# Performance work log

Measured on AMD Instinct MI355X. Metric: run time of the kernel, lower is better.

The kernel has to match this reference:

```python
import jax, jax.numpy as jnp
import numpy as np


def setup_inputs() -> dict:
    key = jax.random.key(0)
    k1, k2, k3, k4, k5 = jax.random.split(key, 5)
    B, ENS, XDIM, YDIM = 8, 256, 8192, 256
    return {
        "Ens_ten": jax.random.normal(k1, (B, ENS, XDIM), dtype=jnp.float32),
        "H": jax.random.normal(k2, (XDIM, YDIM), dtype=jnp.float32),
        "y_true_mean": jax.random.normal(k3, (1, YDIM), dtype=jnp.float32),
        "y_true_std": jax.random.normal(k4, (1, YDIM), dtype=jnp.float32),
        "noise": jax.random.normal(k5, (B, YDIM, ENS), dtype=jnp.float32),
    }


def reference(Ens_ten, H, y_true_mean, y_true_std, noise):
    # Ens_ten: [b, ens, xdim]; H: [xdim, ydim]
    b, ens, xdim = Ens_ten.shape
    Y = jnp.einsum('bex,xy->bey', Ens_ten, H)          # observation_func (linear)
    x_m = jnp.mean(Ens_ten, axis=1, keepdims=True)     # [b,1,xdim]
    y_m = jnp.mean(Y, axis=1, keepdims=True)           # [b,1,ydim]
    Xc = jnp.swapaxes(Ens_ten - x_m, 1, 2)             # [b,xdim,ens]
    Yc = jnp.swapaxes(Y - y_m, 1, 2)                   # [b,ydim,ens]
    C_xy = jnp.einsum('bxe,bye->bxy', Xc, Yc) / ens    # [b,xdim,ydim]
    C_yy = jnp.einsum('bue,bve->buv', Yc, Yc) / ens    # [b,ydim,ydim]
    R = jnp.diag(jnp.square(y_true_std)[0])            # [ydim,ydim], broadcasts over batch
    A = R + C_yy                                       # [b,ydim,ydim]
    # torch.linalg.solve(A, C_xy, left=False): K = C_xy @ inv(A)
    K = jnp.swapaxes(
        jnp.linalg.solve(jnp.swapaxes(A, 1, 2), jnp.swapaxes(C_xy, 1, 2)), 1, 2
    )                                                  # [b,xdim,ydim]
    R_2 = noise * jnp.square(y_true_std)[:, :, None]   # [b,ydim,ens]
    innov = y_true_mean[:, :, None] - Yc + R_2         # [b,ydim,ens]
    update = jnp.einsum('bxy,bye->bxe', K, innov)      # [b,xdim,ens]
    return Ens_ten + jnp.swapaxes(update, 1, 2)
```

## Files before the change

### kernel.cpp

```cpp
#include <hip/hip_runtime.h>

#define ENSN 256
#define XDIM 8192
#define YD 256
#define BATCH 8

#define OFF_Y   0
#define OFF_YC  524288
#define OFF_AUG 1048576
#define OFF_W   2097152
#define OFF_XM  2621440

typedef __attribute__((ext_vector_type(4))) short short4v;
typedef __attribute__((ext_vector_type(8))) short short8v;
typedef __attribute__((ext_vector_type(4))) float float4v;

__device__ __forceinline__ unsigned short f2bf_rne(float x) {
    unsigned u = __float_as_uint(x);
    u += 0x7FFFu + ((u >> 16) & 1u);
    return (unsigned short)(u >> 16);
}

__global__ __launch_bounds__(256) void k1_colmean(const float* __restrict__ E,
                                                  float* __restrict__ xm) {
    int x = blockIdx.x * 256 + threadIdx.x;
    int b = blockIdx.y;
    const float* p = E + (size_t)b * ENSN * XDIM + x;
    float s = 0.f;
    #pragma unroll 8
    for (int e = 0; e < ENSN; e++) s += p[(size_t)e * XDIM];
    xm[b * XDIM + x] = s * (1.0f / ENSN);
}

__global__ __launch_bounds__(256) void kc_h(const float* __restrict__ H,
                                            short* __restrict__ Hthi,
                                            short* __restrict__ Htlo) {
    __shared__ float T[64][65];
    int k0 = blockIdx.x * 64, n0 = blockIdx.y * 64;
    int tid = threadIdx.x;
    int c = tid & 63, g = tid >> 6;
    #pragma unroll
    for (int p = 0; p < 16; p++)
        T[g + p * 4][c] = H[(size_t)(k0 + g + p * 4) * YD + n0 + c];
    __syncthreads();
    #pragma unroll
    for (int p = 0; p < 16; p++) {
        int nn = g + p * 4;
        float v = T[c][nn];
        unsigned short h = f2bf_rne(v);
        float hf = __uint_as_float(((unsigned)h) << 16);
        unsigned short l2 = f2bf_rne(v - hf);
        Hthi[(size_t)(n0 + nn) * XDIM + k0 + c] = (short)h;
        Htlo[(size_t)(n0 + nn) * XDIM + k0 + c] = (short)l2;
    }
}

#define EST 40
#define BST 40

__global__ __launch_bounds__(512, 2) void k2m_ygemm(const float* __restrict__ E,
                                                    const short* __restrict__ Hthi,
                                                    const short* __restrict__ Htlo,
                                                    float* __restrict__ Y) {
    __shared__ __align__(16) short Ehi[64 * EST];
    __shared__ __align__(16) short Elo[64 * EST];
    __shared__ __align__(16) short Bhi[256 * BST];
    __shared__ __align__(16) short Blo[256 * BST];
    int tid = threadIdx.x;
    int lane = tid & 63;
    int w = tid >> 6;
    int m0 = blockIdx.x * 64;
    int kb0 = blockIdx.y * 512;
    int wr = (w & 1) * 32;
    int wc = (w >> 1) * 64;
    float4v acc[8];
    #pragma unroll
    for (int i = 0; i < 8; i++) acc[i] = (float4v){0.f, 0.f, 0.f, 0.f};

    int erow = tid >> 3, ecol = (tid & 7) * 4;
    int brow = tid >> 1, bhalf = (tid & 1) * 16;
    int fr = lane & 15, fg = lane >> 4;

    for (int s = 0; s < 16; s++) {
        int kb = kb0 + s * 32;
        float4 ev = *(const float4*)&E[(size_t)(m0 + erow) * XDIM + kb + ecol];
        float vv[4] = {ev.x, ev.y, ev.z, ev.w};
        short4v hi4, lo4;
        #pragma unroll
        for (int j = 0; j < 4; j++) {
            unsigned short h = f2bf_rne(vv[j]);
            float hf = __uint_as_float(((unsigned)h) << 16);
            unsigned short l2 = f2bf_rne(vv[j] - hf);
            hi4[j] = (short)h; lo4[j] = (short)l2;
        }
        *(short4v*)&Ehi[erow * EST + ecol] = hi4;
        *(short4v*)&Elo[erow * EST + ecol] = lo4;
        short8v bh0 = *(const short8v*)&Hthi[(size_t)brow * XDIM + kb + bhalf];
        short8v bh1 = *(const short8v*)&Hthi[(size_t)brow * XDIM + kb + bhalf + 8];
        short8v bl0 = *(const short8v*)&Htlo[(size_t)brow * XDIM + kb + bhalf];
        short8v bl1 = *(const short8v*)&Htlo[(size_t)brow * XDIM + kb + bhalf + 8];
        *(short8v*)&Bhi[brow * BST + bhalf]     = bh0;
        *(short8v*)&Bhi[brow * BST + bhalf + 8] = bh1;
        *(short8v*)&Blo[brow * BST + bhalf]     = bl0;
        *(short8v*)&Blo[brow * BST + bhalf + 8] = bl1;
        __syncthreads();
        short8v ah[2], al[2], bhf[4], blf[4];
        #pragma unroll
        for (int ti = 0; ti < 2; ti++) {
            ah[ti] = *(const short8v*)&Ehi[(wr + ti * 16 + fr) * EST + fg * 8];
            al[ti] = *(const short8v*)&Elo[(wr + ti * 16 + fr) * EST + fg * 8];
        }
        #pragma unroll
        for (int tj = 0; tj < 4; tj++) {
            bhf[tj] = *(const short8v*)&Bhi[(wc + tj * 16 + fr) * BST + fg * 8];
            blf[tj] = *(const short8v*)&Blo[(wc + tj * 16 + fr) * BST + fg * 8];
        }
        #pragma unroll
        for (int ti = 0; ti < 2; ti++)
            #pragma unroll
            for (int tj = 0; tj < 4; tj++) {
                int a = ti * 4 + tj;
                acc[a] = __builtin_amdgcn_mfma_f32_16x16x32_bf16(ah[ti], bhf[tj], acc[a], 0, 0, 0);
                acc[a] = __builtin_amdgcn_mfma_f32_16x16x32_bf16(ah[ti], blf[tj], acc[a], 0, 0, 0);
                acc[a] = __builtin_amdgcn_mfma_f32_16x16x32_bf16(al[ti], bhf[tj], acc[a], 0, 0, 0);
            }
        __syncthreads();
    }
    #pragma unroll
    for (int ti = 0; ti < 2; ti++)
        #pragma unroll
        for (int tj = 0; tj < 4; tj++)
            #pragma unroll
            for (int q = 0; q < 4; q++) {
                int row = m0 + wr + ti * 16 + fg * 4 + q;
                int col = wc + tj * 16 + fr;
                atomicAdd(&Y[row * YD + col], acc[ti * 4 + tj][q]);
            }
}

__global__ __launch_bounds__(256) void k3_center(const float* __restrict__ Y,
                                                 const float* __restrict__ ytm,
                                                 const float* __restrict__ ystd,
                                                 const float* __restrict__ noise,
                                                 float* __restrict__ Yc,
                                                 float* __restrict__ aug) {
    int b = blockIdx.y, tid = threadIdx.x;
    int y0 = blockIdx.x * 64;
    __shared__ float red[4][64];
    __shared__ float ym[64], tms[64], s2[64];
    __shared__ float T[64][65];
    int yl = tid & 63, q = tid >> 6;
    float s = 0.f;
    for (int e = q * 64; e < q * 64 + 64; e++)
        s += Y[(size_t)(b * ENSN + e) * YD + y0 + yl];
    red[q][yl] = s;
    __syncthreads();
    if (tid < 64) {
        ym[tid] = (red[0][tid] + red[1][tid] + red[2][tid] + red[3][tid]) * (1.0f / ENSN);
        float sd = ystd[y0 + tid];
        s2[tid] = sd * sd;
        tms[tid] = ytm[y0 + tid];
    }
    __syncthreads();
    for (int e0 = 0; e0 < ENSN; e0 += 64) {
        #pragma unroll
        for (int p = 0; p < 16; p++) {
            int er = q + p * 4;
            T[er][yl] = Y[(size_t)(b * ENSN + e0 + er) * YD + y0 + yl];
        }
        __syncthreads();
        int ec = yl;
        #pragma unroll
        for (int p = 0; p < 16; p++) {
            int yr = q + p * 4;
            int y = y0 + yr, e = e0 + ec;
            float yv = T[ec][yr] - ym[yr];
            Yc[(size_t)b * YD * ENSN + (size_t)y * ENSN + e] = yv;
            aug[(size_t)b * YD * 512 + (size_t)y * 512 + 256 + e] =
                tms[yr] - yv + noise[(size_t)b * YD * ENSN + (size_t)y * ENSN + e] * s2[yr];
        }
        __syncthreads();
    }
}

__global__ __launch_bounds__(256) void k4_cyy(const float* __restrict__ Yc,
                                              const float* __restrict__ ystd,
                                              float* __restrict__ aug) {
    __shared__ float As[16][68];
    __shared__ float Bs[16][68];
    int tid = threadIdx.x;
    int m0 = blockIdx.x * 64, n0 = blockIdx.y * 64, b = blockIdx.z;
    const float* Ycb = Yc + (size_t)b * YD * ENSN;
    int tr = tid >> 4, tc = tid & 15;
    float acc[4][4];
    #pragma unroll
    for (int i = 0; i < 4; i++)
        #pragma unroll
        for (int j = 0; j < 4; j++) acc[i][j] = 0.f;
    int al = tid & 15, am0 = tid >> 4;
    for (int k0 = 0; k0 < ENSN; k0 += 16) {
        #pragma unroll
        for (int p = 0; p < 4; p++) {
            int am = am0 + p * 16;
            As[al][am] = Ycb[(m0 + am) * ENSN + k0 + al];
            Bs[al][am] = Ycb[(n0 + am) * ENSN + k0 + al];
        }
        __syncthreads();
        #pragma unroll
        for (int kk = 0; kk < 16; kk++) {
            float4 a = *(const float4*)&As[kk][tr * 4];
            float4 bb = *(const float4*)&Bs[kk][tc * 4];
            float af[4] = {a.x, a.y, a.z, a.w};
            float bf[4] = {bb.x, bb.y, bb.z, bb.w};
            #pragma unroll
            for (int i = 0; i < 4; i++)
                #pragma unroll
                for (int j = 0; j < 4; j++) acc[i][j] += af[i] * bf[j];
        }
        __syncthreads();
    }
    float* augb = aug + (size_t)b * YD * 512;
    #pragma unroll
    for (int i = 0; i < 4; i++) {
        int u = m0 + tr * 4 + i;
        #pragma unroll
        for (int j = 0; j < 4; j++) {
            int v = n0 + tc * 4 + j;
            float val = acc[i][j] * (1.0f / ENSN);
            if (u == v) { float sv = ystd[u]; val += sv * sv; }
            augb[u * 512 + v] = val;
        }
    }
}

#define RSTP 484
#define LSTP 233

__global__ __launch_bounds__(1024, 4) void k5p_panel(float* __restrict__ aug, int c0) {
    __shared__ __align__(16) float R[32 * RSTP];
    __shared__ float Ls[32 * LSTP];
    __shared__ __align__(16) float Dg[32 * 33];
    __shared__ float invd[32];
    int b = blockIdx.x, tid = threadIdx.x;
    float* A = aug + (size_t)b * 256 * 512;
    int r5 = tid >> 5, c5 = tid & 31;
    int WR = 480 - c0;
    int W2 = 224 - c0;

    Dg[r5 * 33 + c5] = A[(c0 + r5) * 512 + c0 + c5];
    __syncthreads();
    if (tid < 32) {
        float u[32];
        #pragma unroll
        for (int c = 0; c < 32; c++) u[c] = Dg[tid * 33 + c];
        for (int j = 0; j < 31; j++) {
            float pv = __shfl(u[j], j);
            float f = u[j] / pv;
            #pragma unroll
            for (int c = 0; c < 32; c++) {
                if (c > j) {
                    float ujc = __shfl(u[c], j);
                    if (tid > j) u[c] -= f * ujc;
                }
            }
            if (tid > j) u[j] = f;
        }
        #pragma unroll
        for (int c = 0; c < 32; c++) Dg[tid * 33 + c] = u[c];
        invd[tid] = 1.0f / u[tid];
    }
    for (int cc = c5; cc < WR; cc += 32)
        R[r5 * RSTP + cc] = A[(c0 + r5) * 512 + c0 + 32 + cc];
    for (int row = r5; row < W2; row += 32)
        Ls[c5 * LSTP + row] = A[(c0 + 32 + row) * 512 + c0 + c5];
    __syncthreads();
    A[(c0 + r5) * 512 + c0 + c5] = Dg[r5 * 33 + c5];
    if (tid < WR) {
        float y[32];
        #pragma unroll
        for (int j = 0; j < 32; j++) {
            float s = R[j * RSTP + tid];
            #pragma unroll
            for (int m = 0; m < 32; m++)
                if (m < j) s -= Dg[j * 33 + m] * y[m];
            y[j] = s;
        }
        #pragma unroll
        for (int j = 0; j < 32; j++)
            A[(c0 + j) * 512 + c0 + 32 + tid] = y[j];
    }
    if (tid >= 512 && tid < 512 + W2) {
        int row = tid - 512;
        float l[32];
        #pragma unroll
        for (int j = 0; j < 32; j++) {
            float s = Ls[j * LSTP + row];
            #pragma unroll
            for (int m = 0; m < 32; m++)
                if (m < j) s -= l[m] * Dg[m * 33 + j];
            l[j] = s * invd[j];
        }
        #pragma unroll
        for (int j = 0; j < 32; j++)
            Ls[j * LSTP + row] = l[j];
    }
    __syncthreads();
    for (int row = r5; row < W2; row += 32)
        A[(c0 + 32 + row) * 512 + c0 + c5] = Ls[c5 * LSTP + row];
}

__global__ __launch_bounds__(256) void k5t_trail(float* __restrict__ aug, int c0) {
    __shared__ __align__(16) float Lt[32][36];
    __shared__ __align__(16) float Ut[32][36];
    int b = blockIdx.z, tid = threadIdx.x;
    float* A = aug + (size_t)b * 256 * 512;
    int r0  = c0 + 32 + blockIdx.x * 32;
    int cc0 = c0 + 32 + blockIdx.y * 32;
    int lr = tid >> 3, lc = (tid & 7) * 4;
    *(float4*)&Lt[lr][lc] = *(const float4*)&A[(size_t)(r0 + lr) * 512 + c0 + lc];
    *(float4*)&Ut[lr][lc] = *(const float4*)&A[(size_t)(c0 + lr) * 512 + cc0 + lc];
    __syncthreads();
    float* gp = &A[(size_t)(r0 + lr) * 512 + cc0 + lc];
    float4 acc = *(const float4*)gp;
    #pragma unroll
    for (int k = 0; k < 32; k++) {
        float lv = Lt[lr][k];
        float4 uv = *(const float4*)&Ut[k][lc];
        acc.x -= lv * uv.x;
        acc.y -= lv * uv.y;
        acc.z -= lv * uv.z;
        acc.w -= lv * uv.w;
    }
    *(float4*)gp = acc;
}

#define ZST  68
#define LBST 36

__global__ __launch_bounds__(512, 2) void k5s_solve(float* __restrict__ aug) {
    __shared__ __align__(16) float Zs[256 * ZST];
    __shared__ __align__(16) float Lb[224 * LBST];
    __shared__ __align__(16) float Dg[32 * 33];
    __shared__ float invd[32];
    int b = blockIdx.y, tid = threadIdx.x;
    float* A = aug + (size_t)b * 256 * 512;
    int cb = blockIdx.x * 64;
    int c = tid & 63, g = tid >> 6;
    int rr = tid >> 5, cc = tid & 31;

    for (int r = g; r < 256; r += 8)
        Zs[r * ZST + c] = A[r * 512 + 256 + cb + c];

    for (int p = 7; p >= 0; p--) {
        int c0 = 32 * p, na = c0;
        for (int r = rr; r < 32; r += 16)
            Dg[r * 33 + cc] = A[(c0 + r) * 512 + c0 + cc];
        for (int r = rr; r < na; r += 16)
            Lb[r * LBST + cc] = A[r * 512 + c0 + cc];
        if (tid < 32)
            invd[tid] = 1.0f / A[(c0 + tid) * 512 + c0 + tid];
        __syncthreads();
        if (tid < 64) {
            float x[32];
            #pragma unroll
            for (int j = 31; j >= 0; j--) {
                float s = Zs[(c0 + j) * ZST + tid];
                #pragma unroll
                for (int m = 0; m < 32; m++)
                    if (m > j) s -= Dg[j * 33 + m] * x[m];
                x[j] = s * invd[j];
            }
            #pragma unroll
            for (int j = 0; j < 32; j++) Zs[(c0 + j) * ZST + tid] = x[j];
        }
        __syncthreads();
        if (na > 0) {
            float z[32];
            #pragma unroll
            for (int k = 0; k < 32; k++) z[k] = Zs[(c0 + k) * ZST + c];
            for (int r = g; r < na; r += 8) {
                const float* lp = &Lb[r * LBST];
                float a0 = 0.f, a1 = 0.f, a2 = 0.f, a3 = 0.f;
                #pragma unroll
                for (int k = 0; k < 32; k += 4) {
                    float4 lv = *(const float4*)(lp + k);
                    a0 += lv.x * z[k + 0];
                    a1 += lv.y * z[k + 1];
                    a2 += lv.z * z[k + 2];
                    a3 += lv.w * z[k + 3];
                }
                Zs[r * ZST + c] -= (a0 + a1) + (a2 + a3);
            }
        }
        __syncthreads();
    }

    for (int r = g; r < 256; r += 8)
        A[r * 512 + 256 + cb + c] = Zs[r * ZST + c];
}

__global__ __launch_bounds__(256) void k6_w(const float* __restrict__ Yc,
                                            const float* __restrict__ aug,
                                            float* __restrict__ W) {
    __shared__ float As[16][68];
    __shared__ float Bs[16][68];
    int tid = threadIdx.x;
    int m0 = blockIdx.x * 64, n0 = blockIdx.y * 64, b = blockIdx.z;
    const float* Ycb = Yc + (size_t)b * YD * ENSN;
    const float* augb = aug + (size_t)b * YD * 512;
    int tr = tid >> 4, tc = tid & 15;
    float acc[4][4];
    #pragma unroll
    for (int i = 0; i < 4; i++)
        #pragma unroll
        for (int j = 0; j < 4; j++) acc[i][j] = 0.f;
    int c = tid & 63, kr0 = tid >> 6;
    for (int k0 = 0; k0 < YD; k0 += 16) {
        #pragma unroll
        for (int p = 0; p < 4; p++) {
            int kk = kr0 + p * 4;
            As[kk][c] = Ycb[(k0 + kk) * ENSN + m0 + c];
            Bs[kk][c] = augb[(k0 + kk) * 512 + 256 + n0 + c];
        }
        __syncthreads();
        #pragma unroll
        for (int kk = 0; kk < 16; kk++) {
            float4 a = *(const float4*)&As[kk][tr * 4];
            float4 bb = *(const float4*)&Bs[kk][tc * 4];
            float af[4] = {a.x, a.y, a.z, a.w};
            float bf[4] = {bb.x, bb.y, bb.z, bb.w};
            #pragma unroll
            for (int i = 0; i < 4; i++)
                #pragma unroll
                for (int j = 0; j < 4; j++) acc[i][j] += af[i] * bf[j];
        }
        __syncthreads();
    }
    float* Wb = W + (size_t)b * ENSN * ENSN;
    #pragma unroll
    for (int i = 0; i < 4; i++)
        #pragma unroll
        for (int j = 0; j < 4; j++)
            Wb[(m0 + tr * 4 + i) * ENSN + n0 + tc * 4 + j] = acc[i][j] * (1.0f / ENSN);
}

__global__ __launch_bounds__(256) void kw_w(const float* __restrict__ W,
                                            short* __restrict__ Wthi,
                                            short* __restrict__ Wtlo) {
    __shared__ float T[64][65];
    int f0 = blockIdx.x * 64, e0 = blockIdx.y * 64, b = blockIdx.z;
    const float* Wb = W + (size_t)b * ENSN * ENSN;
    int tid = threadIdx.x;
    int c = tid & 63, g = tid >> 6;
    #pragma unroll
    for (int p = 0; p < 16; p++)
        T[g + p * 4][c] = Wb[(size_t)(f0 + g + p * 4) * ENSN + e0 + c];
    __syncthreads();
    #pragma unroll
    for (int p = 0; p < 16; p++) {
        int ee = g + p * 4;
        float v = T[c][ee];
        unsigned short h = f2bf_rne(v);
        float hf = __uint_as_float(((unsigned)h) << 16);
        unsigned short l2 = f2bf_rne(v - hf);
        size_t o = (size_t)b * ENSN * ENSN + (size_t)(e0 + ee) * ENSN + f0 + c;
        Wthi[o] = (short)h;
        Wtlo[o] = (short)l2;
    }
}

#define WST 36
#define XST 36

__global__ __launch_bounds__(512, 2) void k7m_update(const float* __restrict__ E,
                                                     const short* __restrict__ Wthi,
                                                     const short* __restrict__ Wtlo,
                                                     const float* __restrict__ xm,
                                                     float* __restrict__ out) {
    __shared__ __align__(16) short Ahi[256 * WST];
    __shared__ __align__(16) short Alo[256 * WST];
    __shared__ __align__(16) short Bhi[64 * XST];
    __shared__ __align__(16) short Blo[64 * XST];
    __shared__ float xs[64];
    int tid = threadIdx.x;
    int lane = tid & 63;
    int w = tid >> 6;
    int x0 = blockIdx.x * 64;
    int b = blockIdx.y;
    const short* Whb = Wthi + (size_t)b * ENSN * ENSN;
    const short* Wlb = Wtlo + (size_t)b * ENSN * ENSN;
    const float* Eb = E + (size_t)b * ENSN * XDIM;
    if (tid < 64) xs[tid] = xm[b * XDIM + x0 + tid];
    __syncthreads();
    int wr = (w & 3) * 64;
    int wc = (w >> 2) * 32;
    float4v acc[8];
    #pragma unroll
    for (int i = 0; i < 8; i++) acc[i] = (float4v){0.f, 0.f, 0.f, 0.f};
    int fr = lane & 15, fg = lane >> 4;
    int ae = tid >> 2, ach = (tid & 3) * 8;
    int bx = tid & 63, bkq = tid >> 6;

    for (int s = 0; s < 8; s++) {
        int k0 = s * 32;
        #pragma unroll
        for (int h = 0; h < 2; h++) {
            int e = ae + h * 128;
            *(short8v*)&Ahi[e * WST + ach] = *(const short8v*)&Whb[(size_t)e * ENSN + k0 + ach];
            *(short8v*)&Alo[e * WST + ach] = *(const short8v*)&Wlb[(size_t)e * ENSN + k0 + ach];
        }
        short4v hi4, lo4;
        #pragma unroll
        for (int j = 0; j < 4; j++) {
            float v = Eb[(size_t)(k0 + bkq * 4 + j) * XDIM + x0 + bx] - xs[bx];
            unsigned short h = f2bf_rne(v);
            float hf = __uint_as_float(((unsigned)h) << 16);
            unsigned short l2 = f2bf_rne(v - hf);
            hi4[j] = (short)h; lo4[j] = (short)l2;
        }
        *(short4v*)&Bhi[bx * XST + bkq * 4] = hi4;
        *(short4v*)&Blo[bx * XST + bkq * 4] = lo4;
        __syncthreads();
        short8v ah[4], al[4], bhf[2], blf[2];
        #pragma unroll
        for (int ti = 0; ti < 4; ti++) {
            ah[ti] = *(const short8v*)&Ahi[(wr + ti * 16 + fr) * WST + fg * 8];
            al[ti] = *(const short8v*)&Alo[(wr + ti * 16 + fr) * WST + fg * 8];
        }
        #pragma unroll
        for (int tj = 0; tj < 2; tj++) {
            bhf[tj] = *(const short8v*)&Bhi[(wc + tj * 16 + fr) * XST + fg * 8];
            blf[tj] = *(const short8v*)&Blo[(wc + tj * 16 + fr) * XST + fg * 8];
        }
        #pragma unroll
        for (int ti = 0; ti < 4; ti++)
            #pragma unroll
            for (int tj = 0; tj < 2; tj++) {
                int a = ti * 2 + tj;
                acc[a] = __builtin_amdgcn_mfma_f32_16x16x32_bf16(ah[ti], bhf[tj], acc[a], 0, 0, 0);
                acc[a] = __builtin_amdgcn_mfma_f32_16x16x32_bf16(ah[ti], blf[tj], acc[a], 0, 0, 0);
                acc[a] = __builtin_amdgcn_mfma_f32_16x16x32_bf16(al[ti], bhf[tj], acc[a], 0, 0, 0);
            }
        __syncthreads();
    }
    #pragma unroll
    for (int ti = 0; ti < 4; ti++)
        #pragma unroll
        for (int tj = 0; tj < 2; tj++)
            #pragma unroll
            for (int q = 0; q < 4; q++) {
                int e = wr + ti * 16 + fg * 4 + q;
                int x = x0 + wc + tj * 16 + fr;
                size_t idx = (size_t)(b * ENSN + e) * XDIM + x;
                out[idx] = E[idx] + acc[ti * 2 + tj][q];
            }
}

extern "C" void kernel_launch(void* const* d_in, const int* in_sizes, int n_in,
                              void* d_out, int out_size, void* d_ws, size_t ws_size,
                              hipStream_t stream) {
    const float* Ens   = (const float*)d_in[0];
    const float* H     = (const float*)d_in[1];
    const float* ytm   = (const float*)d_in[2];
    const float* ystd  = (const float*)d_in[3];
    const float* noise = (const float*)d_in[4];
    float* out = (float*)d_out;
    float* ws  = (float*)d_ws;

    float* Y   = ws + OFF_Y;
    float* Yc  = ws + OFF_YC;
    float* aug = ws + OFF_AUG;
    float* W   = ws + OFF_W;
    float* xm  = ws + OFF_XM;
    short* Hthi = (short*)(ws + 524288);
    short* Htlo = (short*)(ws + 1572864);
    short* Wthi = (short*)(ws + 0);
    short* Wtlo = (short*)(ws + 262144);

    hipMemsetAsync(Y, 0, (size_t)2048 * 256 * sizeof(float), stream);

    k1_colmean<<<dim3(XDIM / 256, BATCH), 256, 0, stream>>>(Ens, xm);
    kc_h<<<dim3(XDIM / 64, YD / 64), 256, 0, stream>>>(H, Hthi, Htlo);
    k2m_ygemm<<<dim3(2048 / 64, 16), 512, 0, stream>>>(Ens, Hthi, Htlo, Y);
    k3_center<<<dim3(4, BATCH), 256, 0, stream>>>(Y, ytm, ystd, noise, Yc, aug);
    k4_cyy<<<dim3(4, 4, BATCH), 256, 0, stream>>>(Yc, ystd, aug);
    for (int p = 0; p < 8; p++) {
        k5p_panel<<<dim3(BATCH), 1024, 0, stream>>>(aug, 32 * p);
        if (p < 7)
            k5t_trail<<<dim3(7 - p, 15 - p, BATCH), 256, 0, stream>>>(aug, 32 * p);
    }
    k5s_solve<<<dim3(4, BATCH), 512, 0, stream>>>(aug);
    k6_w<<<dim3(4, 4, BATCH), 256, 0, stream>>>(Yc, aug, W);
    kw_w<<<dim3(4, 4, BATCH), 256, 0, stream>>>(W, Wthi, Wtlo);
    k7m_update<<<dim3(XDIM / 64, BATCH), 512, 0, stream>>>(Ens, Wthi, Wtlo, xm, out);
}
```

Measured before the change: 697.5 us.

## Precompute inverses of diagonal U blocks to parallelize back-substitution

A new small kernel inverts each 32x32 upper-triangular diagonal block of the LU factor, one block per workgroup. The blocked back-substitution kernel then replaces its serial 64-thread triangular solve with a dense matrix-vector product that uses all 512 threads. This removes a latency-bound serial step from each of the eight panels in exchange for one extra launch and a small amount of extra work. The inverses reuse the W workspace region before W is written, and explicit inversion may slightly change numerical accuracy.

```diff
diff --git a/kernel.cpp b/kernel.cpp
--- a/kernel.cpp
+++ b/kernel.cpp
@@ -334,14 +334,43 @@
     *(float4*)gp = acc;
 }
 
+__global__ __launch_bounds__(64) void k5i_invu(const float* __restrict__ aug,
+                                               float* __restrict__ invU) {
+    __shared__ float Dg[32 * 33];
+    __shared__ float invd[32];
+    int p = blockIdx.x, b = blockIdx.y, tid = threadIdx.x;
+    const float* A = aug + (size_t)b * 256 * 512;
+    int c0 = 32 * p;
+    for (int i = tid; i < 1024; i += 64)
+        Dg[(i >> 5) * 33 + (i & 31)] = A[(size_t)(c0 + (i >> 5)) * 512 + c0 + (i & 31)];
+    __syncthreads();
+    if (tid < 32) invd[tid] = 1.0f / Dg[tid * 33 + tid];
+    __syncthreads();
+    if (tid < 32) {
+        int c = tid;
+        float x[32];
+        #pragma unroll
+        for (int j = 31; j >= 0; j--) {
+            float s = (j == c) ? 1.0f : 0.0f;
+            #pragma unroll
+            for (int m = 0; m < 32; m++)
+                if (m > j) s -= Dg[j * 33 + m] * x[m];
+            x[j] = s * invd[j];
+        }
+        float* op = invU + (size_t)(b * 8 + p) * 1024;
+        #pragma unroll
+        for (int j = 0; j < 32; j++) op[j * 32 + c] = x[j];
+    }
+}
+
 #define ZST  68
 #define LBST 36
 
-__global__ __launch_bounds__(512, 2) void k5s_solve(float* __restrict__ aug) {
+__global__ __launch_bounds__(512, 2) void k5s_solve(float* __restrict__ aug,
+                                                    const float* __restrict__ invU) {
     __shared__ __align__(16) float Zs[256 * ZST];
     __shared__ __align__(16) float Lb[224 * LBST];
     __shared__ __align__(16) float Dg[32 * 33];
-    __shared__ float invd[32];
     int b = blockIdx.y, tid = threadIdx.x;
     float* A = aug + (size_t)b * 256 * 512;
     int cb = blockIdx.x * 64;
@@ -353,41 +382,47 @@
 
     for (int p = 7; p >= 0; p--) {
         int c0 = 32 * p, na = c0;
-        for (int r = rr; r < 32; r += 16)
-            Dg[r * 33 + cc] = A[(c0 + r) * 512 + c0 + cc];
+        for (int i = tid; i < 1024; i += 512)
+            Dg[(i >> 5) * 33 + (i & 31)] = invU[(size_t)(b * 8 + p) * 1024 + i];
         for (int r = rr; r < na; r += 16)
             Lb[r * LBST + cc] = A[r * 512 + c0 + cc];
-        if (tid < 32)
-            invd[tid] = 1.0f / A[(c0 + tid) * 512 + c0 + tid];
-        __syncthreads();
-        if (tid < 64) {
-            float x[32];
-            #pragma unroll
-            for (int j = 31; j >= 0; j--) {
-                float s = Zs[(c0 + j) * ZST + tid];
-                #pragma unroll
-                for (int m = 0; m < 32; m++)
-                    if (m > j) s -= Dg[j * 33 + m] * x[m];
-                x[j] = s * invd[j];
+        __syncthreads();
+        float z[32];
+        #pragma unroll
+        for (int m = 0; m < 32; m++) z[m] = Zs[(c0 + m) * ZST + c];
+        float xr[4];
+        #pragma unroll
+        for (int r4 = 0; r4 < 4; r4++) {
+            const float* dr = &Dg[(g * 4 + r4) * 33];
+            float s0 = 0.f, s1 = 0.f, s2 = 0.f, s3 = 0.f;
+            #pragma unroll
+            for (int m = 0; m < 32; m += 4) {
+                s0 += dr[m + 0] * z[m + 0];
+                s1 += dr[m + 1] * z[m + 1];
+                s2 += dr[m + 2] * z[m + 2];
+                s3 += dr[m + 3] * z[m + 3];
             }
-            #pragma unroll
-            for (int j = 0; j < 32; j++) Zs[(c0 + j) * ZST + tid] = x[j];
-        }
+            xr[r4] = (s0 + s1) + (s2 + s3);
+        }
+        __syncthreads();
+        #pragma unroll
+        for (int r4 = 0; r4 < 4; r4++)
+            Zs[(c0 + g * 4 + r4) * ZST + c] = xr[r4];
         __syncthreads();
         if (na > 0) {
-            float z[32];
-            #pragma unroll
-            for (int k = 0; k < 32; k++) z[k] = Zs[(c0 + k) * ZST + c];
+            float zx[32];
+            #pragma unroll
+            for (int k = 0; k < 32; k++) zx[k] = Zs[(c0 + k) * ZST + c];
             for (int r = g; r < na; r += 8) {
                 const float* lp = &Lb[r * LBST];
                 float a0 = 0.f, a1 = 0.f, a2 = 0.f, a3 = 0.f;
                 #pragma unroll
                 for (int k = 0; k < 32; k += 4) {
                     float4 lv = *(const float4*)(lp + k);
-                    a0 += lv.x * z[k + 0];
-                    a1 += lv.y * z[k + 1];
-                    a2 += lv.z * z[k + 2];
-                    a3 += lv.w * z[k + 3];
+                    a0 += lv.x * zx[k + 0];
+                    a1 += lv.y * zx[k + 1];
+                    a2 += lv.z * zx[k + 2];
+                    a3 += lv.w * zx[k + 3];
                 }
                 Zs[r * ZST + c] -= (a0 + a1) + (a2 + a3);
             }
@@ -576,6 +611,7 @@
     short* Htlo = (short*)(ws + 1572864);
     short* Wthi = (short*)(ws + 0);
     short* Wtlo = (short*)(ws + 262144);
+    float* invU = ws + OFF_W;
 
     hipMemsetAsync(Y, 0, (size_t)2048 * 256 * sizeof(float), stream);
 
@@ -589,7 +625,8 @@
         if (p < 7)
             k5t_trail<<<dim3(7 - p, 15 - p, BATCH), 256, 0, stream>>>(aug, 32 * p);
     }
-    k5s_solve<<<dim3(4, BATCH), 512, 0, stream>>>(aug);
+    k5i_invu<<<dim3(8, BATCH), 64, 0, stream>>>(aug, invU);
+    k5s_solve<<<dim3(4, BATCH), 512, 0, stream>>>(aug, invU);
     k6_w<<<dim3(4, 4, BATCH), 256, 0, stream>>>(Yc, aug, W);
     kw_w<<<dim3(4, 4, BATCH), 256, 0, stream>>>(W, Wthi, Wtlo);
     k7m_update<<<dim3(XDIM / 64, BATCH), 512, 0, stream>>>(Ens, Wthi, Wtlo, xm, out);
```

Result: faster. 658.8 us (-5.5%).
